# Performance work log

Hardware: AMD Instinct MI355X
Metric: run time of the kernel (lower is better)

The kernel has to match this reference:

```python
import jax, jax.numpy as jnp
import numpy as np

NEG_SLOPE = 0.01  # torch nn.LeakyReLU default


def setup_inputs() -> dict:
    key = jax.random.key(0)
    kq, kk, kv, km, kw = jax.random.split(key, 5)
    B, Lq, Lk, Dk, Dv = 4, 2048, 2048, 512, 512
    q = jax.random.normal(kq, (B, Lq, Dk), dtype=jnp.float32)
    k = jax.random.normal(kk, (B, Lk, Dk), dtype=jnp.float32)
    v = jax.random.normal(kv, (B, Lk, Dv), dtype=jnp.float32)
    attn_mask = jax.random.randint(km, (B, Lq, Lk), 0, 2).astype(jnp.int32)
    # xavier_normal for (Dk, 1): std = sqrt(2 / (Dk + 1))
    weight = jax.random.normal(kw, (Dk, 1), dtype=jnp.float32) * np.sqrt(2.0 / (Dk + 1))
    return {"q": q, "k": k, "v": v, "attn_mask": attn_mask, "weight": weight}


def reference(q, k, v, attn_mask, weight):
    # (q - k) @ w  ==  (q @ w) - (k @ w): avoid the [B,Lq,Lk,Dk] intermediate.
    qw = jnp.einsum('bqd,do->bq', q, weight)  # [B, Lq]
    kw = jnp.einsum('bkd,do->bk', k, weight)  # [B, Lk]
    scores = qw[:, :, None] - kw[:, None, :]  # [B, Lq, Lk]
    attn = jnp.where(scores >= 0, scores, NEG_SLOPE * scores)  # LeakyReLU
    masked = attn_mask == 0
    attn = jnp.where(masked, -jnp.inf, attn)
    attn = jax.nn.softmax(attn, axis=2)
    attn = jnp.where(masked, 0.0, attn)
    # dropout omitted (eval mode / identity for reference correctness)
    output = jnp.einsum('bqk,bkd->bqd', attn, v)  # bmm
    return output, attn
```

## Files before the change

### kernel.cpp

```cpp
#include <hip/hip_runtime.h>
#include <math.h>

#define BB 4
#define LQ 2048
#define LK 2048
#define DK 512
#define DV 512

typedef __attribute__((ext_vector_type(8))) _Float16 f16x8;
typedef __attribute__((ext_vector_type(2))) _Float16 f16x2;
typedef __attribute__((ext_vector_type(4))) float f32x4;

#define WS_QW    0
#define WS_KW    8192
#define WS_M     16384
#define WS_INV   24576
#define WS_VF16  32768
#define NOUT     ((size_t)BB * LQ * DV)

__device__ __forceinline__ void lds_barrier() {
    __builtin_amdgcn_sched_barrier(0);
    asm volatile("s_waitcnt lgkmcnt(0)\n\ts_barrier" ::: "memory");
    __builtin_amdgcn_sched_barrier(0);
}

__global__ __launch_bounds__(256) void qkw_kernel(const float* __restrict__ q,
                                                  const float* __restrict__ k,
                                                  const float* __restrict__ w,
                                                  float* __restrict__ ws) {
    int gw   = (int)((blockIdx.x * blockDim.x + threadIdx.x) >> 6);
    int lane = threadIdx.x & 63;
    const int nq = BB * LQ;
    const float* row = (gw < nq) ? (q + (size_t)gw * DK) : (k + (size_t)(gw - nq) * DK);

    float acc = 0.f;
#pragma unroll
    for (int j = 0; j < DK; j += 256) {
        int idx = j + lane * 4;
        float4 rv = *reinterpret_cast<const float4*>(row + idx);
        float4 wv = *reinterpret_cast<const float4*>(w + idx);
        acc += rv.x * wv.x + rv.y * wv.y + rv.z * wv.z + rv.w * wv.w;
    }
#pragma unroll
    for (int off = 32; off >= 1; off >>= 1) acc += __shfl_xor(acc, off, 64);
    if (lane == 0) ws[gw] = acc;
}

__global__ __launch_bounds__(256) void vpack_kernel(const float* __restrict__ v,
                                                    unsigned short* __restrict__ vF) {
    __shared__ float tile[32][517];
    const int k32 = blockIdx.x;
    const int b   = blockIdx.y;
    const int k0  = k32 * 32;
    const int t   = threadIdx.x;

#pragma unroll
    for (int i = 0; i < 16; ++i) {
        int flat = i * 256 + t;
        int row  = flat >> 7;
        int c4   = flat & 127;
        float4 f = *reinterpret_cast<const float4*>(
            v + ((size_t)(b * LK + k0 + row)) * DV + c4 * 4);
        tile[row][c4 * 4 + 0] = f.x;
        tile[row][c4 * 4 + 1] = f.y;
        tile[row][c4 * 4 + 2] = f.z;
        tile[row][c4 * 4 + 3] = f.w;
    }
    __syncthreads();

    const int w = t >> 6, l = t & 63;
    const int rbase = (l >> 4) * 8;
#pragma unroll
    for (int f = 0; f < 8; ++f) {
        int n16 = w * 8 + f;
        int col = n16 * 16 + (l & 15);
        f16x8 vv;
#pragma unroll
        for (int j = 0; j < 8; ++j) vv[j] = (_Float16)tile[rbase + j][col];
        size_t u16base = (((size_t)(b * 32 + n16)) * 64 + k32) * 512;
        *reinterpret_cast<f16x8*>(vF + u16base + l * 8) = vv;
    }
}

__global__ __launch_bounds__(256) void rowstat_kernel(const int* __restrict__ mask,
                                                      float* __restrict__ ws,
                                                      float* __restrict__ attn) {
    __shared__ float kws[LK];
    const int b = (blockIdx.x * 4) / LQ;
    const int t = threadIdx.x;

    const float4* kw4 = reinterpret_cast<const float4*>(ws + WS_KW + b * LK);
#pragma unroll
    for (int i = 0; i < 2; ++i)
        reinterpret_cast<float4*>(kws)[t + i * 256] = kw4[t + i * 256];
    __syncthreads();

    const int wave = t >> 6, lane = t & 63;
    const int rid  = blockIdx.x * 4 + wave;
    const float qwv = ws[WS_QW + rid];
    const int* mrow = mask + (size_t)rid * LK;

    float m = -INFINITY, s = 0.f;
    unsigned int mybits = 0;
#pragma unroll
    for (int i = 0; i < 8; ++i) {
        int e = (i * 64 + lane) * 4;
        int4  mi = *reinterpret_cast<const int4*>(mrow + e);
        float4 kv = reinterpret_cast<const float4*>(kws)[i * 64 + lane];
        float vals[4] = {kv.x, kv.y, kv.z, kv.w};
        int   msks[4] = {mi.x, mi.y, mi.z, mi.w};

        unsigned int bits = (msks[0] ? 1u : 0u) | (msks[1] ? 2u : 0u) |
                            (msks[2] ? 4u : 0u) | (msks[3] ? 8u : 0u);
        mybits |= bits << (i * 4);

#pragma unroll
        for (int j = 0; j < 4; ++j) {
            float sc = qwv - vals[j];
            sc = fmaxf(sc, 0.01f * sc);
            if (msks[j]) {
                if (sc > m) { s = s * __expf(m - sc) + 1.f; m = sc; }
                else        { s += __expf(sc - m); }
            }
        }
    }
#pragma unroll
    for (int off = 32; off >= 1; off >>= 1) {
        float mo = __shfl_xor(m, off, 64);
        float so = __shfl_xor(s, off, 64);
        float M  = fmaxf(m, mo);
        float sa = (m  == M) ? s  : s  * __expf(m  - M);
        float sb = (mo == M) ? so : so * __expf(mo - M);
        m = M; s = sa + sb;
    }
    const float inv = (s > 0.f) ? 1.f / s : 0.f;
    if (lane == 0) {
        ws[WS_M   + rid] = m;
        ws[WS_INV + rid] = inv;
    }

    float* arow = attn + (size_t)rid * LK;
#pragma unroll
    for (int i = 0; i < 8; ++i) {
        float4 kv = reinterpret_cast<const float4*>(kws)[i * 64 + lane];
        float vals[4] = {kv.x, kv.y, kv.z, kv.w};
        unsigned int bits = (mybits >> (i * 4)) & 0xFu;
        float p[4];
#pragma unroll
        for (int j = 0; j < 4; ++j) {
            float sc = qwv - vals[j];
            sc = fmaxf(sc, 0.01f * sc);
            p[j] = (bits & (1u << j)) ? __expf(sc - m) * inv : 0.f;
        }
        *reinterpret_cast<float4*>(arow + (i * 64 + lane) * 4) =
            make_float4(p[0], p[1], p[2], p[3]);
    }
}

__global__ __launch_bounds__(512, 2) void pv_kernel(
        const float* __restrict__ attn,
        const unsigned short* __restrict__ vF,
        float* __restrict__ out) {
    __shared__ unsigned int pH32[2][512];

    const int bid  = blockIdx.x;
    const int xcd  = bid & 7;
    const int rest = bid >> 3;
    const int g    = rest >> 1;
    const int ns   = rest & 1;
    const int u32i = g * 8 + xcd;
    const int b    = u32i >> 6;
    const int ksteps = LK >> 5;

    const int t = threadIdx.x;
    const int w = t >> 6, l = t & 63;
    const bool stager = (t < 128);

    const int row_a = (t >> 6) * 16 + (t & 15);
    const int kb    = ((t >> 4) & 3) * 8;
    const int rid   = u32i * 32 + row_a;
    const float* arow = attn + (size_t)rid * LK + kb;

    const unsigned short* bsrc[2];
#pragma unroll
    for (int nb = 0; nb < 2; ++nb)
        bsrc[nb] = vF + (((size_t)(b * 32 + ns * 16 + w * 2 + nb)) * 64) * 512
                      + (size_t)l * 8;

    auto stage = [&](const float4& x, const float4& y, int buf) {
        unsigned int H[4];
        float f[8] = {x.x, x.y, x.z, x.w, y.x, y.y, y.z, y.w};
#pragma unroll
        for (int jw = 0; jw < 4; ++jw) {
            f16x2 hv;
            hv[0] = (_Float16)f[2 * jw];
            hv[1] = (_Float16)f[2 * jw + 1];
            H[jw] = __builtin_bit_cast(unsigned int, hv);
        }
        *reinterpret_cast<uint4*>(&pH32[buf][t * 4]) = *reinterpret_cast<uint4*>(H);
    };

    f16x8 bC[2], bN[2];
#pragma unroll
    for (int nb = 0; nb < 2; ++nb)
        bC[nb] = *reinterpret_cast<const f16x8*>(bsrc[nb]);

    float4 aCx = {0, 0, 0, 0}, aCy = {0, 0, 0, 0};
    if (stager) {
        float4 x = *reinterpret_cast<const float4*>(arow);
        float4 y = *reinterpret_cast<const float4*>(arow + 4);
        stage(x, y, 0);
        aCx = *reinterpret_cast<const float4*>(arow + 32);
        aCy = *reinterpret_cast<const float4*>(arow + 36);
    }

    f32x4 acc[2][2];
#pragma unroll
    for (int mf = 0; mf < 2; ++mf)
#pragma unroll
        for (int nb = 0; nb < 2; ++nb)
            acc[mf][nb] = (f32x4){0.f, 0.f, 0.f, 0.f};

    lds_barrier();

    for (int s = 0; s < ksteps; ++s) {
        const int buf  = s & 1;
        const int nbuf = buf ^ 1;
        const int sn   = (s + 1 < ksteps) ? s + 1 : s;
        const int sn2  = (s + 2 < ksteps) ? s + 2 : s;

#pragma unroll
        for (int nb = 0; nb < 2; ++nb)
            bN[nb] = *reinterpret_cast<const f16x8*>(bsrc[nb] + (size_t)sn * 512);
        float4 aNx, aNy;
        if (stager) {
            aNx = *reinterpret_cast<const float4*>(arow + sn2 * 32);
            aNy = *reinterpret_cast<const float4*>(arow + sn2 * 32 + 4);
        }

        if (stager) stage(aCx, aCy, nbuf);

        const f16x8* pHf = reinterpret_cast<const f16x8*>(pH32[buf]);
        f16x8 aH[2];
#pragma unroll
        for (int mf = 0; mf < 2; ++mf)
            aH[mf] = pHf[mf * 64 + l];

        __builtin_amdgcn_s_setprio(1);
#pragma unroll
        for (int nb = 0; nb < 2; ++nb)
#pragma unroll
            for (int mf = 0; mf < 2; ++mf)
                acc[mf][nb] = __builtin_amdgcn_mfma_f32_16x16x32_f16(aH[mf], bC[nb], acc[mf][nb], 0, 0, 0);
        __builtin_amdgcn_s_setprio(0);

        lds_barrier();

#pragma unroll
        for (int nb = 0; nb < 2; ++nb) bC[nb] = bN[nb];
        if (stager) { aCx = aNx; aCy = aNy; }
    }

    float* obase = out + ((size_t)u32i * 32) * DV
                       + ns * 256 + w * 32 + (l & 15);
#pragma unroll
    for (int mf = 0; mf < 2; ++mf)
#pragma unroll
        for (int nb = 0; nb < 2; ++nb)
#pragma unroll
            for (int r = 0; r < 4; ++r)
                obase[(size_t)(mf * 16 + (l >> 4) * 4 + r) * DV + nb * 16] = acc[mf][nb][r];
}

extern "C" void kernel_launch(void* const* d_in, const int* in_sizes, int n_in,
                              void* d_out, int out_size, void* d_ws, size_t ws_size,
                              hipStream_t stream) {
    const float* q    = (const float*)d_in[0];
    const float* k    = (const float*)d_in[1];
    const float* v    = (const float*)d_in[2];
    const int*   mask = (const int*)d_in[3];
    const float* w    = (const float*)d_in[4];

    float* out  = (float*)d_out;
    float* attn = out + NOUT;
    float* ws   = (float*)d_ws;

    unsigned short* vF = (unsigned short*)(ws + WS_VF16);

    qkw_kernel<<<4096, 256, 0, stream>>>(q, k, w, ws);
    vpack_kernel<<<dim3(64, 4), 256, 0, stream>>>(v, vF);
    rowstat_kernel<<<2048, 256, 0, stream>>>(mask, ws, attn);
    pv_kernel<<<512, 512, 0, stream>>>(attn, vF, out);
}
```

Before: 75.44 us.

## Emit fp16 attention copy in rowstat and feed PV MFMAs directly from global

The rowstat kernel now also writes an fp16 copy of the attention probabilities to workspace. The PV kernel reads its A operands straight from that copy in MFMA register layout. This removes the fp32 attention re-read, the in-kernel conversion, the LDS staging and the per-step barriers. In exchange rowstat writes 32 MB more, and each PV wave loads its A fragments directly from global, duplicating loads across the 8 waves of a block.

```diff
diff --git a/kernel.cpp b/kernel.cpp
--- a/kernel.cpp
+++ b/kernel.cpp
@@ -16,13 +16,8 @@
 #define WS_M     16384
 #define WS_INV   24576
 #define WS_VF16  32768
+#define WS_PF16  2129920
 #define NOUT     ((size_t)BB * LQ * DV)
-
-__device__ __forceinline__ void lds_barrier() {
-    __builtin_amdgcn_sched_barrier(0);
-    asm volatile("s_waitcnt lgkmcnt(0)\n\ts_barrier" ::: "memory");
-    __builtin_amdgcn_sched_barrier(0);
-}
 
 __global__ __launch_bounds__(256) void qkw_kernel(const float* __restrict__ q,
                                                   const float* __restrict__ k,
@@ -84,7 +79,8 @@
 
 __global__ __launch_bounds__(256) void rowstat_kernel(const int* __restrict__ mask,
                                                       float* __restrict__ ws,
-                                                      float* __restrict__ attn) {
+                                                      float* __restrict__ attn,
+                                                      unsigned short* __restrict__ pf16) {
     __shared__ float kws[LK];
     const int b = (blockIdx.x * 4) / LQ;
     const int t = threadIdx.x;
@@ -140,6 +136,7 @@
     }
 
     float* arow = attn + (size_t)rid * LK;
+    unsigned short* prow = pf16 + (size_t)rid * LK;
 #pragma unroll
     for (int i = 0; i < 8; ++i) {
         float4 kv = reinterpret_cast<const float4*>(kws)[i * 64 + lane];
@@ -152,17 +149,22 @@
             sc = fmaxf(sc, 0.01f * sc);
             p[j] = (bits & (1u << j)) ? __expf(sc - m) * inv : 0.f;
         }
-        *reinterpret_cast<float4*>(arow + (i * 64 + lane) * 4) =
-            make_float4(p[0], p[1], p[2], p[3]);
+        const int k4 = (i * 64 + lane) * 4;
+        *reinterpret_cast<float4*>(arow + k4) = make_float4(p[0], p[1], p[2], p[3]);
+
+        f16x2 h0, h1;
+        h0[0] = (_Float16)p[0]; h0[1] = (_Float16)p[1];
+        h1[0] = (_Float16)p[2]; h1[1] = (_Float16)p[3];
+        *reinterpret_cast<uint2*>(prow + k4) =
+            make_uint2(__builtin_bit_cast(unsigned int, h0),
+                       __builtin_bit_cast(unsigned int, h1));
     }
 }
 
 __global__ __launch_bounds__(512, 2) void pv_kernel(
-        const float* __restrict__ attn,
+        const unsigned short* __restrict__ pf16,
         const unsigned short* __restrict__ vF,
         float* __restrict__ out) {
-    __shared__ unsigned int pH32[2][512];
-
     const int bid  = blockIdx.x;
     const int xcd  = bid & 7;
     const int rest = bid >> 3;
@@ -174,12 +176,12 @@
 
     const int t = threadIdx.x;
     const int w = t >> 6, l = t & 63;
-    const bool stager = (t < 128);
-
-    const int row_a = (t >> 6) * 16 + (t & 15);
-    const int kb    = ((t >> 4) & 3) * 8;
-    const int rid   = u32i * 32 + row_a;
-    const float* arow = attn + (size_t)rid * LK + kb;
+
+    const unsigned short* aptr[2];
+#pragma unroll
+    for (int mf = 0; mf < 2; ++mf)
+        aptr[mf] = pf16 + (size_t)(u32i * 32 + mf * 16 + (l & 15)) * LK
+                        + (l >> 4) * 8;
 
     const unsigned short* bsrc[2];
 #pragma unroll
@@ -187,33 +189,14 @@
         bsrc[nb] = vF + (((size_t)(b * 32 + ns * 16 + w * 2 + nb)) * 64) * 512
                       + (size_t)l * 8;
 
-    auto stage = [&](const float4& x, const float4& y, int buf) {
-        unsigned int H[4];
-        float f[8] = {x.x, x.y, x.z, x.w, y.x, y.y, y.z, y.w};
-#pragma unroll
-        for (int jw = 0; jw < 4; ++jw) {
-            f16x2 hv;
-            hv[0] = (_Float16)f[2 * jw];
-            hv[1] = (_Float16)f[2 * jw + 1];
-            H[jw] = __builtin_bit_cast(unsigned int, hv);
-        }
-        *reinterpret_cast<uint4*>(&pH32[buf][t * 4]) = *reinterpret_cast<uint4*>(H);
-    };
-
-    f16x8 bC[2], bN[2];
+    f16x8 aC[2], aN[2], bC[2], bN[2];
+#pragma unroll
+    for (int mf = 0; mf < 2; ++mf)
+        aC[mf] = *reinterpret_cast<const f16x8*>(aptr[mf]);
 #pragma unroll
     for (int nb = 0; nb < 2; ++nb)
         bC[nb] = *reinterpret_cast<const f16x8*>(bsrc[nb]);
 
-    float4 aCx = {0, 0, 0, 0}, aCy = {0, 0, 0, 0};
-    if (stager) {
-        float4 x = *reinterpret_cast<const float4*>(arow);
-        float4 y = *reinterpret_cast<const float4*>(arow + 4);
-        stage(x, y, 0);
-        aCx = *reinterpret_cast<const float4*>(arow + 32);
-        aCy = *reinterpret_cast<const float4*>(arow + 36);
-    }
-
     f32x4 acc[2][2];
 #pragma unroll
     for (int mf = 0; mf < 2; ++mf)
@@ -221,44 +204,27 @@
         for (int nb = 0; nb < 2; ++nb)
             acc[mf][nb] = (f32x4){0.f, 0.f, 0.f, 0.f};
 
-    lds_barrier();
-
     for (int s = 0; s < ksteps; ++s) {
-        const int buf  = s & 1;
-        const int nbuf = buf ^ 1;
-        const int sn   = (s + 1 < ksteps) ? s + 1 : s;
-        const int sn2  = (s + 2 < ksteps) ? s + 2 : s;
-
+        const int sn = (s + 1 < ksteps) ? s + 1 : s;
+
+#pragma unroll
+        for (int mf = 0; mf < 2; ++mf)
+            aN[mf] = *reinterpret_cast<const f16x8*>(aptr[mf] + sn * 32);
 #pragma unroll
         for (int nb = 0; nb < 2; ++nb)
             bN[nb] = *reinterpret_cast<const f16x8*>(bsrc[nb] + (size_t)sn * 512);
-        float4 aNx, aNy;
-        if (stager) {
-            aNx = *reinterpret_cast<const float4*>(arow + sn2 * 32);
-            aNy = *reinterpret_cast<const float4*>(arow + sn2 * 32 + 4);
-        }
-
-        if (stager) stage(aCx, aCy, nbuf);
-
-        const f16x8* pHf = reinterpret_cast<const f16x8*>(pH32[buf]);
-        f16x8 aH[2];
-#pragma unroll
-        for (int mf = 0; mf < 2; ++mf)
-            aH[mf] = pHf[mf * 64 + l];
-
-        __builtin_amdgcn_s_setprio(1);
+
 #pragma unroll
         for (int nb = 0; nb < 2; ++nb)
 #pragma unroll
             for (int mf = 0; mf < 2; ++mf)
-                acc[mf][nb] = __builtin_amdgcn_mfma_f32_16x16x32_f16(aH[mf], bC[nb], acc[mf][nb], 0, 0, 0);
-        __builtin_amdgcn_s_setprio(0);
-
-        lds_barrier();
-
+                acc[mf][nb] = __builtin_amdgcn_mfma_f32_16x16x32_f16(
+                    aC[mf], bC[nb], acc[mf][nb], 0, 0, 0);
+
+#pragma unroll
+        for (int mf = 0; mf < 2; ++mf) aC[mf] = aN[mf];
 #pragma unroll
         for (int nb = 0; nb < 2; ++nb) bC[nb] = bN[nb];
-        if (stager) { aCx = aNx; aCy = aNy; }
     }
 
     float* obase = out + ((size_t)u32i * 32) * DV
@@ -285,10 +251,11 @@
     float* attn = out + NOUT;
     float* ws   = (float*)d_ws;
 
-    unsigned short* vF = (unsigned short*)(ws + WS_VF16);
+    unsigned short* vF   = (unsigned short*)(ws + WS_VF16);
+    unsigned short* pf16 = (unsigned short*)(ws + WS_PF16);
 
     qkw_kernel<<<4096, 256, 0, stream>>>(q, k, w, ws);
     vpack_kernel<<<dim3(64, 4), 256, 0, stream>>>(v, vF);
-    rowstat_kernel<<<2048, 256, 0, stream>>>(mask, ws, attn);
-    pv_kernel<<<512, 512, 0, stream>>>(attn, vF, out);
-}
+    rowstat_kernel<<<2048, 256, 0, stream>>>(mask, ws, attn, pf16);
+    pv_kernel<<<512, 512, 0, stream>>>(pf16, vF, out);
+}
```

Measured after the change: 116.4 us. 54.3% more time.
